# Performance work log

Measured on AMD Instinct MI355X. Metric: run time of the kernel, lower is better.

## Reference

```python
import jax, jax.numpy as jnp
import numpy as np

DIM = 1024
NHEAD = 16
HEAD_DIM = DIM // NHEAD


def setup_inputs() -> dict:
    key = jax.random.key(0)
    k_x, k_wqkv, k_bqkv, k_wp, k_bp = jax.random.split(key, 5)
    scale = 1.0 / np.sqrt(DIM)
    return {
        "x": jax.random.normal(k_x, (4, 2048, DIM), dtype=jnp.float32),
        "w_qkv": jax.random.uniform(k_wqkv, (DIM, 3 * DIM), minval=-scale, maxval=scale, dtype=jnp.float32),
        "b_qkv": jax.random.uniform(k_bqkv, (3 * DIM,), minval=-scale, maxval=scale, dtype=jnp.float32),
        "w_proj": jax.random.uniform(k_wp, (DIM, DIM), minval=-scale, maxval=scale, dtype=jnp.float32),
        "b_proj": jax.random.uniform(k_bp, (DIM,), minval=-scale, maxval=scale, dtype=jnp.float32),
    }


def reference(x, w_qkv, b_qkv, w_proj, b_proj):
    B, N, D = x.shape
    # qkv projection: [B,N,3D] -> [3,B,H,N,hd]
    qkv = x @ w_qkv + b_qkv
    qkv = qkv.reshape(B, N, 3, NHEAD, HEAD_DIM).transpose(2, 0, 3, 1, 4)
    q, k, v = qkv[0], qkv[1], qkv[2]
    # naive full attention: scores [B,H,N,N]
    attn = jnp.einsum("bhqd,bhkd->bhqk", q, k) / jnp.sqrt(jnp.float32(HEAD_DIM))
    attn = jax.nn.softmax(attn, axis=-1)
    out = jnp.einsum("bhqk,bhkd->bhqd", attn, v)  # [B,H,N,hd]
    out = out.transpose(0, 2, 1, 3).reshape(B, N, D)
    return out @ w_proj + b_proj
```

## Files before the change

### kernel.cpp

```cpp
#include <hip/hip_runtime.h>
#include <math.h>

#define DIM     1024
#define NHEAD   16
#define HD      64
#define BATCH   4
#define SEQ     2048
#define MTOT    (BATCH * SEQ)
#define QKV_N   (3 * DIM)

typedef __attribute__((ext_vector_type(8))) short bf16x8;
typedef __attribute__((ext_vector_type(4))) float f32x4;
typedef unsigned int u32;
typedef unsigned short u16;

__device__ __forceinline__ u16 f2bf(float f) {
    u32 u = __float_as_uint(f);
    return (u16)((u + 0x7fffu + ((u >> 16) & 1u)) >> 16);
}

__device__ __forceinline__ float exp2_fast(float x) {
    float r; asm("v_exp_f32 %0, %1" : "=v"(r) : "v"(x)); return r;
}

__device__ __forceinline__ u32 cvtpk_bf16(float lo, float hi) {
    u32 r; asm("v_cvt_pk_bf16_f32 %0, %1, %2" : "=v"(r) : "v"(lo), "v"(hi));
    return r;
}

__device__ __forceinline__ void gload_lds16(const u16* g, u16* l) {
    __builtin_amdgcn_global_load_lds((const __attribute__((address_space(1))) u32*)g,
                                     (__attribute__((address_space(3))) u32*)l, 16, 0, 0);
}

__global__ __launch_bounds__(256) void prep(
    const float* __restrict__ x,  u16* __restrict__ xb,
    const float* __restrict__ wq, u16* __restrict__ wqt,
    const float* __restrict__ wp, u16* __restrict__ wpt)
{
    const int b = blockIdx.x;
    if (b < 8192) {
        const int i = (b * 256 + threadIdx.x) * 4;
        const float4 v = *(const float4*)&x[i];
        ushort4 o;
        o.x = f2bf(v.x); o.y = f2bf(v.y); o.z = f2bf(v.z); o.w = f2bf(v.w);
        *(ushort4*)&xb[i] = o;
        return;
    }
    __shared__ float Ls[64][65];
    int i = b - 8192;
    const float* W; u16* Wt; int N;
    if (i < 768) { W = wq; Wt = wqt; N = QKV_N; }
    else         { i -= 768; W = wp; Wt = wpt; N = DIM; }
    const int k0 = (i & 15) * 64, n0 = (i >> 4) * 64;
    const int t = threadIdx.x;
    const int r = t >> 4, c4 = (t & 15) << 2;
    #pragma unroll
    for (int j = 0; j < 4; ++j) {
        const float4 v = *(const float4*)&W[(size_t)(k0 + r + j * 16) * N + n0 + c4];
        Ls[r + j * 16][c4 + 0] = v.x; Ls[r + j * 16][c4 + 1] = v.y;
        Ls[r + j * 16][c4 + 2] = v.z; Ls[r + j * 16][c4 + 3] = v.w;
    }
    __syncthreads();
    #pragma unroll
    for (int j = 0; j < 4; ++j) {
        const int nr = r + j * 16;
        ushort4 o;
        o.x = f2bf(Ls[c4 + 0][nr]); o.y = f2bf(Ls[c4 + 1][nr]);
        o.z = f2bf(Ls[c4 + 2][nr]); o.w = f2bf(Ls[c4 + 3][nr]);
        *(ushort4*)&Wt[(size_t)(n0 + nr) * DIM + k0 + c4] = o;
    }
}

#define GEMM_STAGE(buf, kof, Aptr, Bptr)                                       \
    _Pragma("unroll") for (int i = 0; i < 2; ++i) {                            \
        const int row = w * 32 + i * 16 + (lane >> 2);                         \
        const int slot = (lane & 3) ^ ((row >> 1) & 3);                        \
        gload_lds16(&Aptr[(size_t)(m0 + row) * DIM + (kof) + slot * 8],        \
                    &As[buf][(w * 32 + i * 16) * 32]);                         \
        gload_lds16(&Bptr[(size_t)(n0 + row) * DIM + (kof) + slot * 8],        \
                    &Bs[buf][(w * 32 + i * 16) * 32]);                         \
    }

#define GEMM_MAINLOOP(Aptr, Bptr)                                              \
    __shared__ __align__(16) u16 As[2][128 * 32];                              \
    __shared__ __align__(16) u16 Bs[2][128 * 32];                              \
    const int t = threadIdx.x;                                                 \
    const int lane = t & 63, w = t >> 6;                                       \
    const int n0 = blockIdx.x * 128;                                           \
    const int m0 = blockIdx.y * 128;                                           \
    const int wm = (w & 1) * 64, wn = (w >> 1) * 64;                           \
    const int g = lane >> 4, li = lane & 15;                                   \
    f32x4 acc[4][4];                                                           \
    _Pragma("unroll") for (int mt = 0; mt < 4; ++mt)                           \
        _Pragma("unroll") for (int nt = 0; nt < 4; ++nt)                       \
            acc[mt][nt] = (f32x4){0.f, 0.f, 0.f, 0.f};                         \
    GEMM_STAGE(0, 0, Aptr, Bptr)                                               \
    __syncthreads();                                                           \
    int cur = 0;                                                               \
    for (int k0 = 0; k0 < DIM; k0 += 32) {                                     \
        if (k0 + 32 < DIM) { GEMM_STAGE(cur ^ 1, k0 + 32, Aptr, Bptr) }        \
        bf16x8 a[4], b[4];                                                     \
        _Pragma("unroll") for (int mt = 0; mt < 4; ++mt) {                     \
            const int row = wm + mt * 16 + li;                                 \
            const int slot = g ^ ((row >> 1) & 3);                             \
            a[mt] = *(const bf16x8*)&As[cur][row * 32 + slot * 8];             \
        }                                                                      \
        _Pragma("unroll") for (int nt = 0; nt < 4; ++nt) {                     \
            const int row = wn + nt * 16 + li;                                 \
            const int slot = g ^ ((row >> 1) & 3);                             \
            b[nt] = *(const bf16x8*)&Bs[cur][row * 32 + slot * 8];             \
        }                                                                      \
        _Pragma("unroll") for (int mt = 0; mt < 4; ++mt)                       \
            _Pragma("unroll") for (int nt = 0; nt < 4; ++nt)                   \
                acc[mt][nt] = __builtin_amdgcn_mfma_f32_16x16x32_bf16(         \
                    a[mt], b[nt], acc[mt][nt], 0, 0, 0);                       \
        __syncthreads();                                                       \
        cur ^= 1;                                                              \
    }

#define QSCALE 0.18033688011112042f
__global__ __launch_bounds__(256) void gemm_qkv(
    const u16* __restrict__ A, const u16* __restrict__ Bt,
    const float* __restrict__ bias,
    u16* __restrict__ qo, u16* __restrict__ ko, u16* __restrict__ vo)
{
    GEMM_MAINLOOP(A, Bt)
    #pragma unroll
    for (int nt = 0; nt < 4; ++nt) {
        const int n = n0 + wn + nt * 16 + li;
        const int which = n >> 10;
        const int head  = (n >> 6) & 15;
        const int hd    = n & 63;
        u16* dst = (which == 0) ? qo : (which == 1) ? ko : vo;
        const float scale = (which == 0) ? QSCALE : 1.0f;
        const float bv = bias[n];
        #pragma unroll
        for (int mt = 0; mt < 4; ++mt) {
            #pragma unroll
            for (int r = 0; r < 4; ++r) {
                const int m = m0 + wm + mt * 16 + g * 4 + r;
                const int bb = m >> 11, tok = m & 2047;
                dst[((size_t)(bb * NHEAD + head) * SEQ + tok) * HD + hd] =
                    f2bf((acc[mt][nt][r] + bv) * scale);
            }
        }
    }
}

__global__ __launch_bounds__(256) void gemm_proj(
    const u16* __restrict__ A, const u16* __restrict__ Bt,
    const float* __restrict__ bias, float* __restrict__ out)
{
    GEMM_MAINLOOP(A, Bt)
    #pragma unroll
    for (int nt = 0; nt < 4; ++nt) {
        const int n = n0 + wn + nt * 16 + li;
        const float bv = bias[n];
        #pragma unroll
        for (int mt = 0; mt < 4; ++mt) {
            #pragma unroll
            for (int r = 0; r < 4; ++r) {
                const int m = m0 + wm + mt * 16 + g * 4 + r;
                out[(size_t)m * DIM + n] = acc[mt][nt][r] + bv;
            }
        }
    }
}

#define LSTR 72
#define NKT  (SEQ / 64)
__global__ __launch_bounds__(256) void attn_mfma(
    const u16* __restrict__ q, const u16* __restrict__ k,
    const u16* __restrict__ v, u16* __restrict__ ao)
{
    __shared__ __align__(16) u16 Ks[2][64 * LSTR];
    __shared__ __align__(16) u16 Vt[2][64 * LSTR];

    const int t = threadIdx.x;
    const int lane = t & 63, w = t >> 6;
    const int g = lane >> 4, li = lane & 15;
    const int q0 = blockIdx.x * 128;
    const int bh = blockIdx.y;
    const size_t base = (size_t)bh * SEQ * HD;

    bf16x8 qf[2][2];
    #pragma unroll
    for (int h = 0; h < 2; ++h) {
        const size_t qrow = base + (size_t)(q0 + w * 32 + h * 16 + li) * HD;
        qf[h][0] = *(const bf16x8*)&q[qrow + g * 8];
        qf[h][1] = *(const bf16x8*)&q[qrow + 32 + g * 8];
    }

    float lsum[2] = {0.f, 0.f};
    f32x4 oacc[2][4];
    #pragma unroll
    for (int h = 0; h < 2; ++h)
        #pragma unroll
        for (int nt = 0; nt < 4; ++nt) oacc[h][nt] = (f32x4){0.f, 0.f, 0.f, 0.f};

    const int kk = t >> 2, kh = (t & 3) << 4;
    const int kperm = (kk & 32) | (((kk >> 2) & 3) << 3)
                    | (((kk >> 4) & 1) << 2) | (kk & 3);
    const int vkey = (t & 31) << 1, vh0 = (t >> 5) << 3;

    bf16x8 rk0, rk1, rv0, rv1;
    rk0 = *(const bf16x8*)&k[base + (size_t)kperm * HD + kh];
    rk1 = *(const bf16x8*)&k[base + (size_t)kperm * HD + kh + 8];
    rv0 = *(const bf16x8*)&v[base + (size_t)vkey * HD + vh0];
    rv1 = *(const bf16x8*)&v[base + (size_t)(vkey + 1) * HD + vh0];
    {
        u16* Kn = Ks[0]; u16* Vn = Vt[0];
        *(bf16x8*)&Kn[kk * LSTR + kh]     = rk0;
        *(bf16x8*)&Kn[kk * LSTR + kh + 8] = rk1;
        #pragma unroll
        for (int i = 0; i < 8; ++i) {
            const u32 pk = (u32)(u16)rv0[i] | ((u32)(u16)rv1[i] << 16);
            *(u32*)&Vn[(vh0 + i) * LSTR + vkey] = pk;
        }
    }
    __syncthreads();

    int cur = 0;
    for (int kt = 0; kt < NKT; ++kt) {
        const bool more = (kt + 1 < NKT);
        if (more) {
            const size_t kb = base + (size_t)(kt + 1) * 64 * HD;
            rk0 = *(const bf16x8*)&k[kb + (size_t)kperm * HD + kh];
            rk1 = *(const bf16x8*)&k[kb + (size_t)kperm * HD + kh + 8];
            rv0 = *(const bf16x8*)&v[kb + (size_t)vkey * HD + vh0];
            rv1 = *(const bf16x8*)&v[kb + (size_t)(vkey + 1) * HD + vh0];
        }
        const u16* Kc = Ks[cur];
        const u16* Vc = Vt[cur];

        f32x4 s[2][4];
        __builtin_amdgcn_s_setprio(1);
        #pragma unroll
        for (int nt = 0; nt < 4; ++nt) {
            const bf16x8 kf0 = *(const bf16x8*)&Kc[(nt * 16 + li) * LSTR + g * 8];
            const bf16x8 kf1 = *(const bf16x8*)&Kc[(nt * 16 + li) * LSTR + 32 + g * 8];
            #pragma unroll
            for (int h = 0; h < 2; ++h) {
                f32x4 c = (f32x4){0.f, 0.f, 0.f, 0.f};
                c = __builtin_amdgcn_mfma_f32_16x16x32_bf16(kf0, qf[h][0], c, 0, 0, 0);
                c = __builtin_amdgcn_mfma_f32_16x16x32_bf16(kf1, qf[h][1], c, 0, 0, 0);
                s[h][nt] = c;
            }
        }
        __builtin_amdgcn_s_setprio(0);

        bf16x8 pb[2][2];
        #pragma unroll
        for (int h = 0; h < 2; ++h) {
            float rs = 0.f;
            #pragma unroll
            for (int nt = 0; nt < 4; ++nt)
                #pragma unroll
                for (int r = 0; r < 4; ++r) {
                    const float p = exp2_fast(s[h][nt][r]);
                    s[h][nt][r] = p;
                    rs += p;
                }
            lsum[h] += rs;
            #pragma unroll
            for (int ks = 0; ks < 2; ++ks) {
                union { u32 u[4]; bf16x8 v8; } uu;
                uu.u[0] = cvtpk_bf16(s[h][2 * ks][0],     s[h][2 * ks][1]);
                uu.u[1] = cvtpk_bf16(s[h][2 * ks][2],     s[h][2 * ks][3]);
                uu.u[2] = cvtpk_bf16(s[h][2 * ks + 1][0], s[h][2 * ks + 1][1]);
                uu.u[3] = cvtpk_bf16(s[h][2 * ks + 1][2], s[h][2 * ks + 1][3]);
                pb[h][ks] = uu.v8;
            }
        }

        __builtin_amdgcn_s_setprio(1);
        #pragma unroll
        for (int ks = 0; ks < 2; ++ks) {
            #pragma unroll
            for (int nt = 0; nt < 4; ++nt) {
                const bf16x8 vb = *(const bf16x8*)&Vc[(nt * 16 + li) * LSTR + ks * 32 + g * 8];
                #pragma unroll
                for (int h = 0; h < 2; ++h)
                    oacc[h][nt] = __builtin_amdgcn_mfma_f32_16x16x32_bf16(
                        vb, pb[h][ks], oacc[h][nt], 0, 0, 0);
            }
        }
        __builtin_amdgcn_s_setprio(0);

        if (more) {
            u16* Kn = Ks[cur ^ 1]; u16* Vn = Vt[cur ^ 1];
            *(bf16x8*)&Kn[kk * LSTR + kh]     = rk0;
            *(bf16x8*)&Kn[kk * LSTR + kh + 8] = rk1;
            #pragma unroll
            for (int i = 0; i < 8; ++i) {
                const u32 pk = (u32)(u16)rv0[i] | ((u32)(u16)rv1[i] << 16);
                *(u32*)&Vn[(vh0 + i) * LSTR + vkey] = pk;
            }
        }
        __syncthreads();
        cur ^= 1;
    }

    const int bb = bh >> 4, hh = bh & 15;
    #pragma unroll
    for (int h = 0; h < 2; ++h) {
        float lf = lsum[h];
        lf += __shfl_xor(lf, 16);
        lf += __shfl_xor(lf, 32);
        const float inv = 1.0f / lf;
        const int tok = q0 + w * 32 + h * 16 + li;
        u16* dst = &ao[(size_t)(bb * SEQ + tok) * DIM + hh * HD];
        #pragma unroll
        for (int nt = 0; nt < 4; ++nt) {
            const u32 p0 = cvtpk_bf16(oacc[h][nt][0] * inv, oacc[h][nt][1] * inv);
            const u32 p1 = cvtpk_bf16(oacc[h][nt][2] * inv, oacc[h][nt][3] * inv);
            *(u32*)&dst[nt * 16 + g * 4]     = p0;
            *(u32*)&dst[nt * 16 + g * 4 + 2] = p1;
        }
    }
}

extern "C" void kernel_launch(void* const* d_in, const int* in_sizes, int n_in,
                              void* d_out, int out_size, void* d_ws, size_t ws_size,
                              hipStream_t stream)
{
    const float* x      = (const float*)d_in[0];
    const float* w_qkv  = (const float*)d_in[1];
    const float* b_qkv  = (const float*)d_in[2];
    const float* w_proj = (const float*)d_in[3];
    const float* b_proj = (const float*)d_in[4];
    float* out = (float*)d_out;

    u16* xb  = (u16*)d_ws;
    u16* wqt = xb  + (size_t)MTOT * DIM;
    u16* wpt = wqt + (size_t)QKV_N * DIM;
    u16* qb  = wpt + (size_t)DIM * DIM;
    u16* kb  = qb  + (size_t)MTOT * DIM;
    u16* vb  = kb  + (size_t)MTOT * DIM;
    u16* aob = vb  + (size_t)MTOT * DIM;

    prep<<<8192 + 768 + 256, 256, 0, stream>>>(x, xb, w_qkv, wqt, w_proj, wpt);
    gemm_qkv<<<dim3(QKV_N / 128, MTOT / 128), 256, 0, stream>>>(xb, wqt, b_qkv, qb, kb, vb);
    attn_mfma<<<dim3(SEQ / 128, BATCH * NHEAD), 256, 0, stream>>>(qb, kb, vb, aob);
    gemm_proj<<<dim3(DIM / 128, MTOT / 128), 256, 0, stream>>>(aob, wpt, b_proj, out);
}
```

Measured before the change: 204.1 us.

## Double attention block to 256 queries with 512 threads sharing K/V tiles

New measurement: 193.1 us. 1.06x faster.

```diff
diff --git a/kernel.cpp b/kernel.cpp
--- a/kernel.cpp
+++ b/kernel.cpp
@@ -170,7 +170,7 @@
 
 #define LSTR 72
 #define NKT  (SEQ / 64)
-__global__ __launch_bounds__(256) void attn_mfma(
+__global__ __launch_bounds__(512) void attn_mfma(
     const u16* __restrict__ q, const u16* __restrict__ k,
     const u16* __restrict__ v, u16* __restrict__ ao)
 {
@@ -180,7 +180,7 @@
     const int t = threadIdx.x;
     const int lane = t & 63, w = t >> 6;
     const int g = lane >> 4, li = lane & 15;
-    const int q0 = blockIdx.x * 128;
+    const int q0 = blockIdx.x * 256;
     const int bh = blockIdx.y;
     const size_t base = (size_t)bh * SEQ * HD;
 
@@ -199,25 +199,26 @@
         #pragma unroll
         for (int nt = 0; nt < 4; ++nt) oacc[h][nt] = (f32x4){0.f, 0.f, 0.f, 0.f};
 
-    const int kk = t >> 2, kh = (t & 3) << 4;
+    const int kk = t >> 3;
+    const int kh = (t & 7) << 3;
     const int kperm = (kk & 32) | (((kk >> 2) & 3) << 3)
                     | (((kk >> 4) & 1) << 2) | (kk & 3);
-    const int vkey = (t & 31) << 1, vh0 = (t >> 5) << 3;
-
-    bf16x8 rk0, rk1, rv0, rv1;
-    rk0 = *(const bf16x8*)&k[base + (size_t)kperm * HD + kh];
-    rk1 = *(const bf16x8*)&k[base + (size_t)kperm * HD + kh + 8];
-    rv0 = *(const bf16x8*)&v[base + (size_t)vkey * HD + vh0];
-    rv1 = *(const bf16x8*)&v[base + (size_t)(vkey + 1) * HD + vh0];
+    const int vkp = (t & 31) << 1;
+    const int vh0 = (t >> 5) << 2;
+
+    bf16x8 rk;
+    ushort4 rv0, rv1;
+    rk  = *(const bf16x8*)&k[base + (size_t)kperm * HD + kh];
+    rv0 = *(const ushort4*)&v[base + (size_t)vkp * HD + vh0];
+    rv1 = *(const ushort4*)&v[base + (size_t)(vkp + 1) * HD + vh0];
     {
         u16* Kn = Ks[0]; u16* Vn = Vt[0];
-        *(bf16x8*)&Kn[kk * LSTR + kh]     = rk0;
-        *(bf16x8*)&Kn[kk * LSTR + kh + 8] = rk1;
-        #pragma unroll
-        for (int i = 0; i < 8; ++i) {
-            const u32 pk = (u32)(u16)rv0[i] | ((u32)(u16)rv1[i] << 16);
-            *(u32*)&Vn[(vh0 + i) * LSTR + vkey] = pk;
-        }
+        *(bf16x8*)&Kn[kk * LSTR + kh] = rk;
+        const u16 a0[4] = {rv0.x, rv0.y, rv0.z, rv0.w};
+        const u16 b0[4] = {rv1.x, rv1.y, rv1.z, rv1.w};
+        #pragma unroll
+        for (int i = 0; i < 4; ++i)
+            *(u32*)&Vn[(vh0 + i) * LSTR + vkp] = (u32)a0[i] | ((u32)b0[i] << 16);
     }
     __syncthreads();
 
@@ -226,10 +227,9 @@
         const bool more = (kt + 1 < NKT);
         if (more) {
             const size_t kb = base + (size_t)(kt + 1) * 64 * HD;
-            rk0 = *(const bf16x8*)&k[kb + (size_t)kperm * HD + kh];
-            rk1 = *(const bf16x8*)&k[kb + (size_t)kperm * HD + kh + 8];
-            rv0 = *(const bf16x8*)&v[kb + (size_t)vkey * HD + vh0];
-            rv1 = *(const bf16x8*)&v[kb + (size_t)(vkey + 1) * HD + vh0];
+            rk  = *(const bf16x8*)&k[kb + (size_t)kperm * HD + kh];
+            rv0 = *(const ushort4*)&v[kb + (size_t)vkp * HD + vh0];
+            rv1 = *(const ushort4*)&v[kb + (size_t)(vkp + 1) * HD + vh0];
         }
         const u16* Kc = Ks[cur];
         const u16* Vc = Vt[cur];
@@ -290,13 +290,12 @@
 
         if (more) {
             u16* Kn = Ks[cur ^ 1]; u16* Vn = Vt[cur ^ 1];
-            *(bf16x8*)&Kn[kk * LSTR + kh]     = rk0;
-            *(bf16x8*)&Kn[kk * LSTR + kh + 8] = rk1;
-            #pragma unroll
-            for (int i = 0; i < 8; ++i) {
-                const u32 pk = (u32)(u16)rv0[i] | ((u32)(u16)rv1[i] << 16);
-                *(u32*)&Vn[(vh0 + i) * LSTR + vkey] = pk;
-            }
+            *(bf16x8*)&Kn[kk * LSTR + kh] = rk;
+            const u16 a0[4] = {rv0.x, rv0.y, rv0.z, rv0.w};
+            const u16 b0[4] = {rv1.x, rv1.y, rv1.z, rv1.w};
+            #pragma unroll
+            for (int i = 0; i < 4; ++i)
+                *(u32*)&Vn[(vh0 + i) * LSTR + vkp] = (u32)a0[i] | ((u32)b0[i] << 16);
         }
         __syncthreads();
         cur ^= 1;
@@ -342,6 +341,6 @@
 
     prep<<<8192 + 768 + 256, 256, 0, stream>>>(x, xb, w_qkv, wqt, w_proj, wpt);
     gemm_qkv<<<dim3(QKV_N / 128, MTOT / 128), 256, 0, stream>>>(xb, wqt, b_qkv, qb, kb, vb);
-    attn_mfma<<<dim3(SEQ / 128, BATCH * NHEAD), 256, 0, stream>>>(qb, kb, vb, aob);
+    attn_mfma<<<dim3(SEQ / 256, BATCH * NHEAD), 512, 0, stream>>>(qb, kb, vb, aob);
     gemm_proj<<<dim3(DIM / 128, MTOT / 128), 256, 0, stream>>>(aob, wpt, b_proj, out);
 }
```
